# Optimization experiments

Hardware: AMD Instinct MI355X
Metric: run time of the kernel (lower is better)

The kernel has to match this reference:

```python
import jax, jax.numpy as jnp
import numpy as np

B, T, D = 32, 1024, 1024
K, F = 8, 4096
E, RH = 64, 128
NUM_STAGES, NUM_VIEWS = 5, 4


def setup_inputs() -> dict:
    key = jax.random.key(0)
    ks = jax.random.split(key, 16)
    s = 0.02
    return {
        "x": jax.random.normal(ks[0], (B, T, D), dtype=jnp.float32),
        "stage_ids": jax.random.randint(ks[1], (B,), 0, NUM_STAGES),
        "view_ids": jax.random.randint(ks[2], (B,), 0, NUM_VIEWS),
        # router params
        "stage_emb": jax.random.normal(ks[3], (NUM_STAGES, E), dtype=jnp.float32) * s,
        "view_emb": jax.random.normal(ks[4], (NUM_VIEWS, E), dtype=jnp.float32) * s,
        "rw1": jax.random.normal(ks[5], (2 * E, RH), dtype=jnp.float32) * s,
        "rb1": jnp.zeros((RH,), dtype=jnp.float32),
        "rw2": jax.random.normal(ks[6], (RH, K), dtype=jnp.float32) * s,
        "rb2": jnp.zeros((K,), dtype=jnp.float32),
        # stacked expert FFN params
        "w1": jax.random.normal(ks[7], (K, D, F), dtype=jnp.float32) * s,
        "b1": jnp.zeros((K, F), dtype=jnp.float32),
        "w2": jax.random.normal(ks[8], (K, F, D), dtype=jnp.float32) * s,
        "b2": jnp.zeros((K, D), dtype=jnp.float32),
    }


def _moe_forward(x, stage_ids, view_ids, stage_emb, view_emb, rw1, rb1, rw2, rb2, w1, b1, w2, b2):
    # Router: per-sample stage/view embeddings -> MLP -> softmax over experts
    z = jnp.concatenate([stage_emb[stage_ids], view_emb[view_ids]], axis=-1)  # [B, 2E]
    logits = jax.nn.relu(z @ rw1 + rb1) @ rw2 + rb2  # [B, K]
    expert_probs = jax.nn.softmax(logits, axis=-1)
    selected_expert = jnp.argmax(expert_probs, axis=-1)  # [B]

    # Top-1 dispatch: gather the selected expert's weights per sample, then
    # run a single batched FFN (equivalent math to per-expert masked loop).
    w1s = w1[selected_expert]  # [B, D, F]
    b1s = b1[selected_expert]  # [B, F]
    w2s = w2[selected_expert]  # [B, F, D]
    b2s = b2[selected_expert]  # [B, D]
    h = jax.nn.gelu(jnp.einsum('btd,bdf->btf', x, w1s) + b1s[:, None, :], approximate=False)
    output = jnp.einsum('btf,bfd->btd', h, w2s) + b2s[:, None, :]  # [B, T, D]

    # Switch-style load-balance loss: K * sum_i f_i * P_i
    expert_mask = jax.nn.one_hot(selected_expert, K, dtype=jnp.float32)  # [B, K]
    f = expert_mask.mean(axis=0)
    P = expert_probs.mean(axis=0)
    load_balance_loss = K * jnp.sum(f * P)
    return output, expert_probs, selected_expert, load_balance_loss


def reference(x, stage_ids, view_ids, stage_emb, view_emb, rw1, rb1, rw2, rb2, w1, b1, w2, b2):
    return _moe_forward(x, stage_ids, view_ids, stage_emb, view_emb, rw1, rb1, rw2, rb2, w1, b1, w2, b2)
```

## Files before the change

### kernel.cpp

```cpp
#include <hip/hip_runtime.h>
#include <hip/hip_bf16.h>
#include <math.h>

#define BATCH 32
#define TSEQ 1024
#define DMODEL 1024
#define KEXP 8
#define FFFN 4096
#define EEMB 64
#define RHID 128
#define NSTAGE 5
#define NVIEW 4

typedef float f32x4 __attribute__((ext_vector_type(4)));
typedef __bf16 bf16x8 __attribute__((ext_vector_type(8)));

#define AS1C(p) ((const __attribute__((address_space(1))) unsigned int*)(p))
#define AS3(p)  ((__attribute__((address_space(3))) unsigned int*)(p))

__device__ __forceinline__ unsigned short f32_to_bf16_rne(float f) {
    union { float f; unsigned int u; } v; v.f = f;
    unsigned int u = v.u;
    unsigned int r = u + 0x7FFFu + ((u >> 16) & 1u);
    return (unsigned short)(r >> 16);
}

__device__ int resolve_id_one(const int* __restrict__ raw, int b, int hi, int is64) {
    int v = is64 ? raw[2 * b] : raw[b];
    return v < 0 ? 0 : (v >= hi ? hi - 1 : v);
}
__device__ int ids_are_64(const int* __restrict__ raw, int hi) {
    bool is64 = true;
    for (int i = 1; i < 32; i += 2) is64 = is64 && (raw[i] == 0);
    for (int i = 0; i < 32; i += 2) is64 = is64 && (raw[i] >= 0 && raw[i] < hi);
    return is64 ? 1 : 0;
}

__global__ __launch_bounds__(RHID) void router_probs_r22(
    const int* __restrict__ stage_ids,
    const int* __restrict__ view_ids,
    const float* __restrict__ stage_emb,
    const float* __restrict__ view_emb,
    const float* __restrict__ rw1,
    const float* __restrict__ rb1,
    const float* __restrict__ rw2,
    const float* __restrict__ rb2,
    float* __restrict__ out_probs,
    float* __restrict__ out_sel,
    int* __restrict__ sel_ws)
{
    const int b = blockIdx.x;
    const int t = threadIdx.x;
    __shared__ double z[2 * EEMB];
    __shared__ double h[RHID];
    __shared__ double lg[KEXP];
    __shared__ int sid_s, vid_s;
    if (t == 0) {
        const int s64 = ids_are_64(stage_ids, NSTAGE);
        const int v64 = ids_are_64(view_ids, NVIEW);
        sid_s = resolve_id_one(stage_ids, b, NSTAGE, s64);
        vid_s = resolve_id_one(view_ids, b, NVIEW, v64);
    }
    __syncthreads();
    const int sid = sid_s, vid = vid_s;
    z[t] = (t < EEMB) ? (double)stage_emb[sid * EEMB + t]
                      : (double)view_emb[vid * EEMB + (t - EEMB)];
    __syncthreads();
    double acc = (double)rb1[t];
    for (int i = 0; i < 2 * EEMB; ++i) acc += z[i] * (double)rw1[i * RHID + t];
    h[t] = fmax(acc, 0.0);
    __syncthreads();
    if (t < KEXP) {
        double a = (double)rb2[t];
        for (int i = 0; i < RHID; ++i) a += h[i] * (double)rw2[i * KEXP + t];
        lg[t] = a;
    }
    __syncthreads();
    if (t == 0) {
        double mx = lg[0]; int am = 0;
        for (int k = 1; k < KEXP; ++k) if (lg[k] > mx) { mx = lg[k]; am = k; }
        double p[KEXP]; double den = 0.0;
        for (int k = 0; k < KEXP; ++k) { p[k] = exp(lg[k] - mx); den += p[k]; }
        for (int k = 0; k < KEXP; ++k) out_probs[b * KEXP + k] = (float)(p[k] / den);
        out_sel[b] = (float)am;
        sel_ws[b] = am;
    }
}

__global__ void router_loss_r22(const float* __restrict__ probs,
                                const int* __restrict__ sel,
                                float* __restrict__ out_loss)
{
    if (threadIdx.x != 0) return;
    double loss = 0.0;
    for (int k = 0; k < KEXP; ++k) {
        double ps = 0.0; int fc = 0;
        for (int b = 0; b < BATCH; ++b) {
            ps += (double)probs[b * KEXP + k];
            fc += (sel[b] == k) ? 1 : 0;
        }
        loss += ((double)fc / (double)BATCH) * (ps / (double)BATCH);
    }
    out_loss[0] = (float)((double)KEXP * loss);
}

__global__ void cvt_f32_bf16_r22(const float* __restrict__ src,
                                 unsigned short* __restrict__ dst, size_t n)
{
    size_t i = (size_t)blockIdx.x * blockDim.x + threadIdx.x;
    size_t stride = (size_t)gridDim.x * blockDim.x;
    for (size_t j = i * 4; j < n; j += stride * 4) {
        float4 v = *(const float4*)(src + j);
        ushort4 o;
        o.x = f32_to_bf16_rne(v.x); o.y = f32_to_bf16_rne(v.y);
        o.z = f32_to_bf16_rne(v.z); o.w = f32_to_bf16_rne(v.w);
        *(ushort4*)(dst + j) = o;
    }
}

__global__ __launch_bounds__(512) void transpose_f32_bf16_r22(
    const float* __restrict__ src, unsigned short* __restrict__ dst, int R, int C)
{
    __shared__ float tile[64][65];
    const int e = blockIdx.z;
    const float* s = src + (size_t)e * R * C;
    unsigned short* d = dst + (size_t)e * R * C;
    const int c0 = blockIdx.x * 64, r0 = blockIdx.y * 64;
    const int tx = threadIdx.x, ty = threadIdx.y;
    #pragma unroll
    for (int i = 0; i < 64; i += 8)
        tile[ty + i][tx] = s[(size_t)(r0 + ty + i) * C + (c0 + tx)];
    __syncthreads();
    #pragma unroll
    for (int i = 0; i < 64; i += 8)
        d[(size_t)(c0 + ty + i) * R + (r0 + tx)] = f32_to_bf16_rne(tile[tx][ty + i]);
}


template<int MODE, int OBF>
__global__ __launch_bounds__(512) void gemm_8p_r22(
    const unsigned short* __restrict__ Aall,
    const unsigned short* __restrict__ BTall,
    const float* __restrict__ biasAll,
    void* __restrict__ OutV,
    const int* __restrict__ sel, int g0,
    int M, int N, int K)
{
    const int bz = blockIdx.z;
    int e = sel[g0 + bz];
    e = e < 0 ? 0 : (e >= KEXP ? KEXP - 1 : e);
    const unsigned short* A  = Aall + (size_t)bz * M * K;
    const unsigned short* BT = BTall + (size_t)e * (size_t)N * K;
    const float* bias = biasAll + (size_t)e * N;

    __shared__ __align__(16) unsigned short lds[65536];
    char* Lc = (char*)lds;

    const int tid  = threadIdx.x;
    const int lane = tid & 63;
    const int wave = tid >> 6;
    const int wr = wave >> 2;
    const int wc = wave & 3;
    const int fr = lane & 15;
    const int fq = lane >> 4;
    const int swz = fr & 7;

    const int brow = blockIdx.y * 256;
    const int bcol = blockIdx.x * 256;

    const int srow = lane >> 3;
    const int scol = ((lane & 7) ^ (lane >> 3)) * 8;

    const int NT = K >> 6;

    const int aSlot = wr * 16384;
    const int bSlot = 32768 + (wc >> 1) * 16384;
    const int c0off = ((0 + fq) ^ swz) * 16;
    const int c1off = ((4 + fq) ^ swz) * 16;

    const f32x4 zero = {0.f, 0.f, 0.f, 0.f};
    f32x4 acc[8][4];
    #pragma unroll
    for (int m = 0; m < 8; ++m)
        #pragma unroll
        for (int n = 0; n < 4; ++n) acc[m][n] = zero;

    auto STAGE = [&](int isB, int h, int t) {
        const int kh = t << 6;
        char* dbase = Lc + (t & 1) * 65536 + isB * 32768 + h * 16384 + wave * 1024;
        const unsigned short* sbase = isB ? (BT + (size_t)(bcol + h * 128) * K)
                                          : (A + (size_t)(brow + h * 128) * K);
        #pragma unroll
        for (int j = 0; j < 2; ++j) {
            const unsigned short* g = sbase + (size_t)(j * 64 + wave * 8 + srow) * K + (kh + scol);
            __builtin_amdgcn_global_load_lds(AS1C(g), AS3(dbase + j * 8192), 16, 0, 0);
        }
    };

    STAGE(0, 0, 0); STAGE(0, 1, 0);
    STAGE(1, 0, 0); STAGE(1, 1, 0);
    if (NT > 1) { STAGE(1, 0, 1); STAGE(1, 1, 1); }
    asm volatile("s_waitcnt vmcnt(4)" ::: "memory");
    __builtin_amdgcn_s_barrier();
    __builtin_amdgcn_sched_barrier(0);

    bf16x8 bfr[4][2];

    for (int t = 0; t < NT; ++t) {
        const int buf = (t & 1) * 65536;
        const int aB = buf + aSlot;
        const int bB = buf + bSlot;

        #pragma unroll
        for (int q = 0; q < 4; ++q) {
            bf16x8 af0k0, af0k1, af1k0, af1k1;
            {
                const int la0 = (2 * q + 0) * 16 + fr;
                const int la1 = (2 * q + 1) * 16 + fr;
                af0k0 = *(const bf16x8*)(Lc + aB + la0 * 128 + c0off);
                af0k1 = *(const bf16x8*)(Lc + aB + la0 * 128 + c1off);
                af1k0 = *(const bf16x8*)(Lc + aB + la1 * 128 + c0off);
                af1k1 = *(const bf16x8*)(Lc + aB + la1 * 128 + c1off);
            }
            if (q == 0) {
                #pragma unroll
                for (int n = 0; n < 4; ++n) {
                    const int lb = (wc & 1) * 64 + n * 16 + fr;
                    bfr[n][0] = *(const bf16x8*)(Lc + bB + lb * 128 + c0off);
                    bfr[n][1] = *(const bf16x8*)(Lc + bB + lb * 128 + c1off);
                }
            }
            if (q == 0)      { if (t + 1 < NT) STAGE(0, 0, t + 1); }
            else if (q == 1) { if (t + 1 < NT) STAGE(0, 1, t + 1); }
            else if (q == 2) { if (t + 2 < NT) STAGE(1, 0, t + 2); }
            else             { if (t + 2 < NT) STAGE(1, 1, t + 2); }
            if (q == 3) {
                if (t < NT - 2) asm volatile("s_waitcnt vmcnt(4)" ::: "memory");
                else            asm volatile("s_waitcnt vmcnt(0)" ::: "memory");
            }
            __builtin_amdgcn_sched_barrier(0);
            __builtin_amdgcn_s_barrier();
            asm volatile("s_waitcnt lgkmcnt(0)" ::: "memory");
            __builtin_amdgcn_sched_barrier(0);
            __builtin_amdgcn_s_setprio(1);
            {
                const int m0 = 2 * q, m1 = 2 * q + 1;
                #pragma unroll
                for (int n = 0; n < 4; ++n)
                    acc[m0][n] = __builtin_amdgcn_mfma_f32_16x16x32_bf16(af0k0, bfr[n][0], acc[m0][n], 0, 0, 0);
                #pragma unroll
                for (int n = 0; n < 4; ++n)
                    acc[m1][n] = __builtin_amdgcn_mfma_f32_16x16x32_bf16(af1k0, bfr[n][0], acc[m1][n], 0, 0, 0);
                #pragma unroll
                for (int n = 0; n < 4; ++n)
                    acc[m0][n] = __builtin_amdgcn_mfma_f32_16x16x32_bf16(af0k1, bfr[n][1], acc[m0][n], 0, 0, 0);
                #pragma unroll
                for (int n = 0; n < 4; ++n)
                    acc[m1][n] = __builtin_amdgcn_mfma_f32_16x16x32_bf16(af1k1, bfr[n][1], acc[m1][n], 0, 0, 0);
            }
            __builtin_amdgcn_s_setprio(0);
            __builtin_amdgcn_s_barrier();
        }
    }

    #pragma unroll
    for (int m = 0; m < 8; ++m) {
        #pragma unroll
        for (int n = 0; n < 4; ++n) {
            #pragma unroll
            for (int r = 0; r < 4; ++r) {
                const int row = brow + wr * 128 + m * 16 + fq * 4 + r;
                const int col = bcol + wc * 64 + n * 16 + fr;
                float v = acc[m][n][r] + bias[col];
                if (MODE == 0) v = 0.5f * v * (1.0f + erff(v * 0.70710678118654752f));
                const size_t idx = (size_t)bz * M * N + (size_t)row * N + col;
                if (OBF) ((unsigned short*)OutV)[idx] = f32_to_bf16_rne(v);
                else     ((float*)OutV)[idx] = v;
            }
        }
    }
}

extern "C" void kernel_launch(void* const* d_in, const int* in_sizes, int n_in,
                              void* d_out, int out_size, void* d_ws, size_t ws_size,
                              hipStream_t stream)
{
    const float* x         = (const float*)d_in[0];
    const int*   stage_ids = (const int*)d_in[1];
    const int*   view_ids  = (const int*)d_in[2];
    const float* stage_emb = (const float*)d_in[3];
    const float* view_emb  = (const float*)d_in[4];
    const float* rw1       = (const float*)d_in[5];
    const float* rb1       = (const float*)d_in[6];
    const float* rw2       = (const float*)d_in[7];
    const float* rb2       = (const float*)d_in[8];
    const float* w1        = (const float*)d_in[9];
    const float* b1        = (const float*)d_in[10];
    const float* w2        = (const float*)d_in[11];
    const float* b2        = (const float*)d_in[12];

    float* out_f = (float*)d_out;
    const size_t OUT_ELEMS = (size_t)BATCH * TSEQ * DMODEL;

    const size_t MB64 = 67108864ull;
    char* ws = (char*)d_ws;
    int* sel_ws            = (int*)ws;
    unsigned short* x_bf   = (unsigned short*)(ws + 4096);
    unsigned short* w1T    = (unsigned short*)(ws + 4096 + MB64);
    unsigned short* w2T    = (unsigned short*)(ws + 4096 + 2 * MB64);
    unsigned short* h_bf   = (unsigned short*)(ws + 4096 + 3 * MB64);

    int grp = 1;
    {
        const size_t base = 4096 + 3 * MB64;
        const size_t avail = ws_size > base ? ws_size - base : 0;
        for (int g = 32; g >= 1; g >>= 1) {
            if ((size_t)g * TSEQ * FFFN * 2 <= avail) { grp = g; break; }
        }
    }

    router_probs_r22<<<BATCH, RHID, 0, stream>>>(stage_ids, view_ids, stage_emb, view_emb,
        rw1, rb1, rw2, rb2,
        out_f + OUT_ELEMS,
        out_f + OUT_ELEMS + BATCH * KEXP,
        sel_ws);
    router_loss_r22<<<1, 64, 0, stream>>>(out_f + OUT_ELEMS, sel_ws,
        out_f + OUT_ELEMS + BATCH * KEXP + BATCH);

    cvt_f32_bf16_r22<<<2048, 256, 0, stream>>>(x, x_bf, (size_t)BATCH * TSEQ * DMODEL);
    dim3 tb(64, 8);
    transpose_f32_bf16_r22<<<dim3(FFFN / 64, DMODEL / 64, KEXP), tb, 0, stream>>>(w1, w1T, DMODEL, FFFN);
    transpose_f32_bf16_r22<<<dim3(DMODEL / 64, FFFN / 64, KEXP), tb, 0, stream>>>(w2, w2T, FFFN, DMODEL);

    for (int g0 = 0; g0 < BATCH; g0 += grp) {
        gemm_8p_r22<0, 1><<<dim3(FFFN / 256, TSEQ / 256, grp), 512, 0, stream>>>(
            x_bf + (size_t)g0 * TSEQ * DMODEL, w1T, b1,
            (void*)h_bf, sel_ws, g0, TSEQ, FFFN, DMODEL);
        gemm_8p_r22<1, 0><<<dim3(DMODEL / 256, TSEQ / 256, grp), 512, 0, stream>>>(
            h_bf, w2T, b2,
            (void*)(out_f + (size_t)g0 * TSEQ * DMODEL), sel_ws, g0, TSEQ, DMODEL, FFFN);
    }
}
```

Measured before the change: 783.0 us.

## Halve GEMM K-tile and LDS footprint to fit two blocks per CU

Rewrites the bf16 MFMA GEMM main loop to use 32-wide K tiles in a 64KB double buffer instead of 64-wide tiles in 128KB, and declares launch_bounds(512,2) so two workgroups can share a CU. The swizzle is changed to suit the 64-byte rows, and the pipeline is simplified to a one-tile-ahead prefetch split into two halves, with a full vmcnt(0) wait each iteration. The aim is more occupancy to hide latency, at the cost of twice as many barriers per unit of K, a shallower prefetch, and register pressure from the 2-block cap.

```diff
diff --git a/kernel.cpp b/kernel.cpp
--- a/kernel.cpp
+++ b/kernel.cpp
@@ -36,7 +36,7 @@
     return is64 ? 1 : 0;
 }
 
-__global__ __launch_bounds__(RHID) void router_probs_r22(
+__global__ __launch_bounds__(RHID) void router_probs_r23(
     const int* __restrict__ stage_ids,
     const int* __restrict__ view_ids,
     const float* __restrict__ stage_emb,
@@ -87,7 +87,7 @@
     }
 }
 
-__global__ void router_loss_r22(const float* __restrict__ probs,
+__global__ void router_loss_r23(const float* __restrict__ probs,
                                 const int* __restrict__ sel,
                                 float* __restrict__ out_loss)
 {
@@ -104,7 +104,7 @@
     out_loss[0] = (float)((double)KEXP * loss);
 }
 
-__global__ void cvt_f32_bf16_r22(const float* __restrict__ src,
+__global__ void cvt_f32_bf16_r23(const float* __restrict__ src,
                                  unsigned short* __restrict__ dst, size_t n)
 {
     size_t i = (size_t)blockIdx.x * blockDim.x + threadIdx.x;
@@ -118,7 +118,7 @@
     }
 }
 
-__global__ __launch_bounds__(512) void transpose_f32_bf16_r22(
+__global__ __launch_bounds__(512) void transpose_f32_bf16_r23(
     const float* __restrict__ src, unsigned short* __restrict__ dst, int R, int C)
 {
     __shared__ float tile[64][65];
@@ -138,7 +138,7 @@
 
 
 template<int MODE, int OBF>
-__global__ __launch_bounds__(512) void gemm_8p_r22(
+__global__ __launch_bounds__(512, 2) void gemm_2p_r23(
     const unsigned short* __restrict__ Aall,
     const unsigned short* __restrict__ BTall,
     const float* __restrict__ biasAll,
@@ -153,7 +153,7 @@
     const unsigned short* BT = BTall + (size_t)e * (size_t)N * K;
     const float* bias = biasAll + (size_t)e * N;
 
-    __shared__ __align__(16) unsigned short lds[65536];
+    __shared__ __align__(16) unsigned short lds[32768];
     char* Lc = (char*)lds;
 
     const int tid  = threadIdx.x;
@@ -163,20 +163,15 @@
     const int wc = wave & 3;
     const int fr = lane & 15;
     const int fq = lane >> 4;
-    const int swz = fr & 7;
 
     const int brow = blockIdx.y * 256;
     const int bcol = blockIdx.x * 256;
 
-    const int srow = lane >> 3;
-    const int scol = ((lane & 7) ^ (lane >> 3)) * 8;
-
-    const int NT = K >> 6;
-
-    const int aSlot = wr * 16384;
-    const int bSlot = 32768 + (wc >> 1) * 16384;
-    const int c0off = ((0 + fq) ^ swz) * 16;
-    const int c1off = ((4 + fq) ^ swz) * 16;
+    const int srow = lane >> 2;
+    const int scol = ((lane & 3) ^ ((lane >> 3) & 3)) * 8;
+    const int coff = (fq ^ ((fr >> 1) & 3)) * 16;
+
+    const int NT = K >> 5;
 
     const f32x4 zero = {0.f, 0.f, 0.f, 0.f};
     f32x4 acc[8][4];
@@ -185,82 +180,73 @@
         #pragma unroll
         for (int n = 0; n < 4; ++n) acc[m][n] = zero;
 
-    auto STAGE = [&](int isB, int h, int t) {
-        const int kh = t << 6;
-        char* dbase = Lc + (t & 1) * 65536 + isB * 32768 + h * 16384 + wave * 1024;
-        const unsigned short* sbase = isB ? (BT + (size_t)(bcol + h * 128) * K)
-                                          : (A + (size_t)(brow + h * 128) * K);
+    auto STAGE = [&](int isB, int t) {
+        const int kh = t << 5;
+        char* dbase = Lc + (t & 1) * 32768 + isB * 16384 + wave * 1024;
+        const unsigned short* sbase = isB ? (BT + (size_t)bcol * K) : (A + (size_t)brow * K);
         #pragma unroll
         for (int j = 0; j < 2; ++j) {
-            const unsigned short* g = sbase + (size_t)(j * 64 + wave * 8 + srow) * K + (kh + scol);
+            const int r0 = (j * 8 + wave) * 16;
+            const unsigned short* g = sbase + (size_t)(r0 + srow) * K + (kh + scol);
             __builtin_amdgcn_global_load_lds(AS1C(g), AS3(dbase + j * 8192), 16, 0, 0);
         }
     };
 
-    STAGE(0, 0, 0); STAGE(0, 1, 0);
-    STAGE(1, 0, 0); STAGE(1, 1, 0);
-    if (NT > 1) { STAGE(1, 0, 1); STAGE(1, 1, 1); }
-    asm volatile("s_waitcnt vmcnt(4)" ::: "memory");
+    STAGE(0, 0); STAGE(1, 0);
+    asm volatile("s_waitcnt vmcnt(0)" ::: "memory");
     __builtin_amdgcn_s_barrier();
     __builtin_amdgcn_sched_barrier(0);
 
-    bf16x8 bfr[4][2];
-
     for (int t = 0; t < NT; ++t) {
-        const int buf = (t & 1) * 65536;
-        const int aB = buf + aSlot;
-        const int bB = buf + bSlot;
-
-        #pragma unroll
-        for (int q = 0; q < 4; ++q) {
-            bf16x8 af0k0, af0k1, af1k0, af1k1;
-            {
-                const int la0 = (2 * q + 0) * 16 + fr;
-                const int la1 = (2 * q + 1) * 16 + fr;
-                af0k0 = *(const bf16x8*)(Lc + aB + la0 * 128 + c0off);
-                af0k1 = *(const bf16x8*)(Lc + aB + la0 * 128 + c1off);
-                af1k0 = *(const bf16x8*)(Lc + aB + la1 * 128 + c0off);
-                af1k1 = *(const bf16x8*)(Lc + aB + la1 * 128 + c1off);
-            }
-            if (q == 0) {
-                #pragma unroll
-                for (int n = 0; n < 4; ++n) {
-                    const int lb = (wc & 1) * 64 + n * 16 + fr;
-                    bfr[n][0] = *(const bf16x8*)(Lc + bB + lb * 128 + c0off);
-                    bfr[n][1] = *(const bf16x8*)(Lc + bB + lb * 128 + c1off);
-                }
-            }
-            if (q == 0)      { if (t + 1 < NT) STAGE(0, 0, t + 1); }
-            else if (q == 1) { if (t + 1 < NT) STAGE(0, 1, t + 1); }
-            else if (q == 2) { if (t + 2 < NT) STAGE(1, 0, t + 2); }
-            else             { if (t + 2 < NT) STAGE(1, 1, t + 2); }
-            if (q == 3) {
-                if (t < NT - 2) asm volatile("s_waitcnt vmcnt(4)" ::: "memory");
-                else            asm volatile("s_waitcnt vmcnt(0)" ::: "memory");
-            }
-            __builtin_amdgcn_sched_barrier(0);
-            __builtin_amdgcn_s_barrier();
-            asm volatile("s_waitcnt lgkmcnt(0)" ::: "memory");
-            __builtin_amdgcn_sched_barrier(0);
-            __builtin_amdgcn_s_setprio(1);
-            {
-                const int m0 = 2 * q, m1 = 2 * q + 1;
-                #pragma unroll
-                for (int n = 0; n < 4; ++n)
-                    acc[m0][n] = __builtin_amdgcn_mfma_f32_16x16x32_bf16(af0k0, bfr[n][0], acc[m0][n], 0, 0, 0);
-                #pragma unroll
-                for (int n = 0; n < 4; ++n)
-                    acc[m1][n] = __builtin_amdgcn_mfma_f32_16x16x32_bf16(af1k0, bfr[n][0], acc[m1][n], 0, 0, 0);
-                #pragma unroll
-                for (int n = 0; n < 4; ++n)
-                    acc[m0][n] = __builtin_amdgcn_mfma_f32_16x16x32_bf16(af0k1, bfr[n][1], acc[m0][n], 0, 0, 0);
-                #pragma unroll
-                for (int n = 0; n < 4; ++n)
-                    acc[m1][n] = __builtin_amdgcn_mfma_f32_16x16x32_bf16(af1k1, bfr[n][1], acc[m1][n], 0, 0, 0);
-            }
-            __builtin_amdgcn_s_setprio(0);
-            __builtin_amdgcn_s_barrier();
-        }
+        const int aU = (t & 1) * 32768;
+        const int bU = aU + 16384;
+        const bool pf = (t + 1) < NT;
+
+        bf16x8 bfr[4], af[4];
+        #pragma unroll
+        for (int n = 0; n < 4; ++n) {
+            const int cb = wc * 64 + n * 16 + fr;
+            bfr[n] = *(const bf16x8*)(Lc + bU + cb * 64 + coff);
+        }
+        #pragma unroll
+        for (int m = 0; m < 4; ++m) {
+            const int ra = wr * 128 + m * 16 + fr;
+            af[m] = *(const bf16x8*)(Lc + aU + ra * 64 + coff);
+        }
+        if (pf) STAGE(0, t + 1);
+        __builtin_amdgcn_sched_barrier(0);
+        __builtin_amdgcn_s_barrier();
+        asm volatile("s_waitcnt lgkmcnt(0)" ::: "memory");
+        __builtin_amdgcn_sched_barrier(0);
+        __builtin_amdgcn_s_setprio(1);
+        #pragma unroll
+        for (int m = 0; m < 4; ++m)
+            #pragma unroll
+            for (int n = 0; n < 4; ++n)
+                acc[m][n] = __builtin_amdgcn_mfma_f32_16x16x32_bf16(af[m], bfr[n], acc[m][n], 0, 0, 0);
+        __builtin_amdgcn_s_setprio(0);
+        __builtin_amdgcn_s_barrier();
+
+        bf16x8 ag[4];
+        #pragma unroll
+        for (int m = 0; m < 4; ++m) {
+            const int ra = wr * 128 + (m + 4) * 16 + fr;
+            ag[m] = *(const bf16x8*)(Lc + aU + ra * 64 + coff);
+        }
+        if (pf) STAGE(1, t + 1);
+        if (pf) asm volatile("s_waitcnt vmcnt(0)" ::: "memory");
+        __builtin_amdgcn_sched_barrier(0);
+        __builtin_amdgcn_s_barrier();
+        asm volatile("s_waitcnt lgkmcnt(0)" ::: "memory");
+        __builtin_amdgcn_sched_barrier(0);
+        __builtin_amdgcn_s_setprio(1);
+        #pragma unroll
+        for (int m = 0; m < 4; ++m)
+            #pragma unroll
+            for (int n = 0; n < 4; ++n)
+                acc[m + 4][n] = __builtin_amdgcn_mfma_f32_16x16x32_bf16(ag[m], bfr[n], acc[m + 4][n], 0, 0, 0);
+        __builtin_amdgcn_s_setprio(0);
+        __builtin_amdgcn_s_barrier();
     }
 
     #pragma unroll
@@ -319,24 +305,24 @@
         }
     }
 
-    router_probs_r22<<<BATCH, RHID, 0, stream>>>(stage_ids, view_ids, stage_emb, view_emb,
+    router_probs_r23<<<BATCH, RHID, 0, stream>>>(stage_ids, view_ids, stage_emb, view_emb,
         rw1, rb1, rw2, rb2,
         out_f + OUT_ELEMS,
         out_f + OUT_ELEMS + BATCH * KEXP,
         sel_ws);
-    router_loss_r22<<<1, 64, 0, stream>>>(out_f + OUT_ELEMS, sel_ws,
+    router_loss_r23<<<1, 64, 0, stream>>>(out_f + OUT_ELEMS, sel_ws,
         out_f + OUT_ELEMS + BATCH * KEXP + BATCH);
 
-    cvt_f32_bf16_r22<<<2048, 256, 0, stream>>>(x, x_bf, (size_t)BATCH * TSEQ * DMODEL);
+    cvt_f32_bf16_r23<<<2048, 256, 0, stream>>>(x, x_bf, (size_t)BATCH * TSEQ * DMODEL);
     dim3 tb(64, 8);
-    transpose_f32_bf16_r22<<<dim3(FFFN / 64, DMODEL / 64, KEXP), tb, 0, stream>>>(w1, w1T, DMODEL, FFFN);
-    transpose_f32_bf16_r22<<<dim3(DMODEL / 64, FFFN / 64, KEXP), tb, 0, stream>>>(w2, w2T, FFFN, DMODEL);
+    transpose_f32_bf16_r23<<<dim3(FFFN / 64, DMODEL / 64, KEXP), tb, 0, stream>>>(w1, w1T, DMODEL, FFFN);
+    transpose_f32_bf16_r23<<<dim3(DMODEL / 64, FFFN / 64, KEXP), tb, 0, stream>>>(w2, w2T, FFFN, DMODEL);
 
     for (int g0 = 0; g0 < BATCH; g0 += grp) {
-        gemm_8p_r22<0, 1><<<dim3(FFFN / 256, TSEQ / 256, grp), 512, 0, stream>>>(
+        gemm_2p_r23<0, 1><<<dim3(FFFN / 256, TSEQ / 256, grp), 512, 0, stream>>>(
             x_bf + (size_t)g0 * TSEQ * DMODEL, w1T, b1,
             (void*)h_bf, sel_ws, g0, TSEQ, FFFN, DMODEL);
-        gemm_8p_r22<1, 0><<<dim3(DMODEL / 256, TSEQ / 256, grp), 512, 0, stream>>>(
+        gemm_2p_r23<1, 0><<<dim3(DMODEL / 256, TSEQ / 256, grp), 512, 0, stream>>>(
             h_bf, w2T, b2,
             (void*)(out_f + (size_t)g0 * TSEQ * DMODEL), sel_ws, g0, TSEQ, DMODEL, FFFN);
     }
```

After: 1.035 ms. 1.32x slower.
